# Kernel tuning notes

Hardware: AMD Instinct MI355X
Metric: run time of the kernel (lower is better)

Reference implementation:

```python
import jax, jax.numpy as jnp
import numpy as np

I, H, B, T = 5, 256, 4096, 256


def _lstm_layer(x, w_ih, w_hh, b_ih, b_hh):
    # x: [B, T, in]; precompute the input-side gate GEMM for all timesteps
    xg = jnp.einsum('bti,gi->btg', x, w_ih) + b_ih + b_hh  # [B, T, 4H]
    h0 = jnp.zeros((x.shape[0], H), x.dtype)
    c0 = jnp.zeros((x.shape[0], H), x.dtype)

    def step(carry, xg_t):
        h, c = carry
        g = xg_t + h @ w_hh.T                      # [B, 4H]
        i_g, f_g, g_g, o_g = jnp.split(g, 4, axis=-1)  # torch gate order i,f,g,o
        c = jax.nn.sigmoid(f_g) * c + jax.nn.sigmoid(i_g) * jnp.tanh(g_g)
        h = jax.nn.sigmoid(o_g) * jnp.tanh(c)
        return (h, c), h

    (_, _), hs = jax.lax.scan(step, (h0, c0), jnp.swapaxes(xg, 0, 1))  # hs: [T, B, H]
    return jnp.swapaxes(hs, 0, 1)  # [B, T, H]


def setup_inputs() -> dict:
    key = jax.random.key(0)
    ks = jax.random.split(key, 12)
    s = 1.0 / np.sqrt(H)
    u = lambda k, shape: jax.random.uniform(k, shape, jnp.float32, -s, s)
    return {
        'x': jax.random.normal(ks[0], (B, T, I), jnp.float32),
        'w_ih0': u(ks[1], (4 * H, I)),
        'w_hh0': u(ks[2], (4 * H, H)),
        'b_ih0': u(ks[3], (4 * H,)),
        'b_hh0': u(ks[4], (4 * H,)),
        'w_ih1': u(ks[5], (4 * H, H)),
        'w_hh1': u(ks[6], (4 * H, H)),
        'b_ih1': u(ks[7], (4 * H,)),
        'b_hh1': u(ks[8], (4 * H,)),
        'fc_w': u(ks[9], (1, H)),
        'fc_b': u(ks[10], (1,)),
    }


def reference(x, w_ih0, w_hh0, b_ih0, b_hh0, w_ih1, w_hh1, b_ih1, b_hh1, fc_w, fc_b):
    h1 = _lstm_layer(x, w_ih0, w_hh0, b_ih0, b_hh0)   # [B, T, H]
    # dropout between layers is identity in eval mode
    h2 = _lstm_layer(h1, w_ih1, w_hh1, b_ih1, b_hh1)  # [B, T, H]
    out = jnp.einsum('bth,oh->bto', h2, fc_w) + fc_b  # [B, T, 1]
    return out
```

## Files before the change

### kernel.cpp

```cpp
#include <hip/hip_runtime.h>

typedef unsigned short u16;
typedef _Float16 f16_t;
typedef f16_t f16x8 __attribute__((ext_vector_type(8)));
typedef float f32x4 __attribute__((ext_vector_type(4)));
typedef unsigned u32x4 __attribute__((ext_vector_type(4)));

#define T_STEPS 256
#define IN_DIM  5
#define NBLK    256

#define WS_BIAS 1638400
#define WS_FC   1646592
#define WS_GX   1654784
#define GXS     524288
#define WS_CNT  (WS_GX + 8388608)

__device__ __forceinline__ float sigf(float x)  { return 1.0f / (1.0f + __expf(-x)); }
__device__ __forceinline__ float tanh_f(float x){ return 1.0f - 2.0f / (__expf(2.0f * x) + 1.0f); }

__global__ void prep_kernel(const float* __restrict__ wih0, const float* __restrict__ whh0,
                            const float* __restrict__ wih1, const float* __restrict__ whh1,
                            const float* __restrict__ bih0, const float* __restrict__ bhh0,
                            const float* __restrict__ bih1, const float* __restrict__ bhh1,
                            const float* __restrict__ fcw,
                            u16* __restrict__ wsw, float* __restrict__ biases,
                            u16* __restrict__ wsfc, unsigned* __restrict__ cnt)
{
    int j = blockIdx.x * blockDim.x + threadIdx.x;
    if (j < 102400) {
        int slice = j / 3200;
        int rem   = j - slice * 3200;
        int f     = rem >> 6;
        int lane  = rem & 63;
        int sub = slice >> 2, wv = slice & 3;
        int lrow = lane & 15;
        int kp = (lane >> 4) * 8;
        int nt, ks; bool g0;
        if (f < 18) { g0 = true;  nt = f / 9;  ks = f - nt * 9; }
        else        { int ff = f - 18; g0 = false; nt = ff >> 4; ks = ff & 15; }
        int wr = (nt * 2 + (lrow >> 3)) * 256 + sub * 32 + wv * 8 + (lrow & 7);
        u16 tmp[8];
#pragma unroll
        for (int e = 0; e < 8; ++e) {
            int k = kp + e;
            float v;
            if (g0) {
                v = (ks < 8) ? whh0[wr * 256 + ks * 32 + k]
                             : (k < IN_DIM ? wih0[wr * IN_DIM + k] : 0.0f);
            } else {
                v = (ks < 8) ? wih1[wr * 256 + ks * 32 + k]
                             : whh1[wr * 256 + (ks - 8) * 32 + k];
            }
            tmp[e] = __builtin_bit_cast(u16, (f16_t)v);
        }
        *(uint4*)(wsw + (size_t)j * 8) = *(uint4*)tmp;
    } else if (j < 103424) {
        int i = j - 102400;
        biases[i] = bih0[i] + bhh0[i];
    } else if (j < 104448) {
        int i = j - 103424;
        biases[1024 + i] = bih1[i] + bhh1[i];
    } else if (j < 104960) {
        int q = j - 104448;
        int ks = q >> 6, lane = q & 63;
        u16 tmp[8];
#pragma unroll
        for (int e = 0; e < 8; ++e) {
            float v = ((lane & 15) == 0) ? fcw[ks * 32 + (lane >> 4) * 8 + e] : 0.0f;
            tmp[e] = __builtin_bit_cast(u16, (f16_t)v);
        }
        *(uint4*)(wsfc + (size_t)q * 8) = *(uint4*)tmp;
    } else if (j < 107008) {
        cnt[j - 104960] = 0u;
    }
}

__global__ __launch_bounds__(256, 1) void lstm_fused(
    const float* __restrict__ x, const u16* __restrict__ wsw,
    const float* __restrict__ biases, const u16* __restrict__ wsfc,
    const float* __restrict__ fcb_g, float* __restrict__ out,
    u16* __restrict__ gxbase, unsigned* __restrict__ cnt)
{
    extern __shared__ char smem[];
    char* h0A = smem;
    char* h1A = smem + 32768;
    char* xbA = smem + 65536;
    char* h0B = smem + 69632;
    char* h1B = smem + 102400;
    char* xbB = smem + 135168;

    const int tid  = threadIdx.x;
    const int wv   = tid >> 6;
    const int lane = tid & 63;
    const int lrow = lane & 15;
    const int lkg  = lane >> 4;
    const int hf   = lrow >> 3;
    const int cj   = lrow & 7;
    const int sub  = blockIdx.x >> 5;
    const int grp  = blockIdx.x & 31;
    const int r0   = grp * 128;
    const int aswz = (lrow & 7) << 4;
    const int xswz = (lrow & 3) << 4;

    f16x8 w0[2][9], w1[2][16], wfc[8];
    const u16* wbase = wsw + (size_t)(sub * 4 + wv) * 25600;
#pragma unroll
    for (int nt = 0; nt < 2; ++nt)
#pragma unroll
        for (int ks = 0; ks < 9; ++ks) {
            w0[nt][ks] = *(const f16x8*)(wbase + (nt * 9 + ks) * 512 + lane * 8);
            asm volatile("" : "+a"(w0[nt][ks]));
            __builtin_amdgcn_sched_barrier(0);
        }
#pragma unroll
    for (int nt = 0; nt < 2; ++nt)
#pragma unroll
        for (int ks = 0; ks < 16; ++ks) {
            w1[nt][ks] = *(const f16x8*)(wbase + (18 + nt * 16 + ks) * 512 + lane * 8);
            asm volatile("" : "+a"(w1[nt][ks]));
            __builtin_amdgcn_sched_barrier(0);
        }
#pragma unroll
    for (int ks = 0; ks < 8; ++ks) {
        wfc[ks] = *(const f16x8*)(wsfc + ks * 512 + lane * 8);
        asm volatile("" : "+a"(wfc[ks]));
        __builtin_amdgcn_sched_barrier(0);
    }

    float b0[2], b1[2];
#pragma unroll
    for (int nt = 0; nt < 2; ++nt) {
        int wr = (nt * 2 + hf) * 256 + sub * 32 + wv * 8 + cj;
        b0[nt] = biases[wr];
        b1[nt] = biases[1024 + wr];
    }
    const float fcb = fcb_g[0];

    unsigned* cA = cnt + grp * 16;
    unsigned* cB = cnt + 1024 + grp * 16;

    auto gxr = [&](int stream, int which, int parity) -> u16* {
        return gxbase + (size_t)((stream * 2 + which) * 2 + parity) * GXS + grp * 16384;
    };

    for (int i = tid; i < 139264 / 4; i += 256) ((unsigned*)smem)[i] = 0u;
    __syncthreads();
    {
        int i0 = tid, i1 = tid + 256;
        if (i0 < 320) { int row = i0 / 5, k = i0 - row * 5;
            float v = x[((size_t)(r0 + row) * T_STEPS + 0) * IN_DIM + k];
            *(u16*)(xbA + row * 64 + ((2 * k) ^ ((row & 3) << 4))) = __builtin_bit_cast(u16, (f16_t)v); }
        if (i1 < 320) { int row = i1 / 5, k = i1 - row * 5;
            float v = x[((size_t)(r0 + row) * T_STEPS + 0) * IN_DIM + k];
            *(u16*)(xbA + row * 64 + ((2 * k) ^ ((row & 3) << 4))) = __builtin_bit_cast(u16, (f16_t)v); }
    }
    __syncthreads();

    float c0A[4][2] = {}, c1A[4][2] = {}, c0B[4][2] = {}, c1B[4][2] = {};

    auto PUB = [&](u16* gxw, int mt, unsigned hv) {
        unsigned sh = __shfl_xor(hv, 1);
        int rowb = mt * 16 + lkg * 4 + hf * 2;
        unsigned word;
        if (cj & 1) { word = (sh >> 16) | (hv & 0xffff0000u); rowb += 1; }
        else        { word = (hv & 0xffffu) | (sh << 16); }
        int colp = wv * 8 + (cj & ~1);
        *(volatile unsigned*)((char*)gxw + sub * 4096 + rowb * 64 + colp * 2) = word;
    };

    auto GEMM0 = [&](const char* h0s, const char* xbs, float (&cs)[4][2], u16* gxw) {
#pragma unroll
        for (int mt = 0; mt < 4; ++mt) {
            f32x4 a0 = {}, a1 = {};
            const int arow = mt * 16 + lrow;
#pragma unroll
            for (int ks = 0; ks < 8; ++ks) {
                f16x8 a = *(const f16x8*)(h0s + arow * 512 + ((ks * 64 + lkg * 16) ^ aswz));
                a0 = __builtin_amdgcn_mfma_f32_16x16x32_f16(a, w0[0][ks], a0, 0, 0, 0);
                a1 = __builtin_amdgcn_mfma_f32_16x16x32_f16(a, w0[1][ks], a1, 0, 0, 0);
            }
            {
                f16x8 a = *(const f16x8*)(xbs + arow * 64 + ((lkg * 16) ^ xswz));
                a0 = __builtin_amdgcn_mfma_f32_16x16x32_f16(a, w0[0][8], a0, 0, 0, 0);
                a1 = __builtin_amdgcn_mfma_f32_16x16x32_f16(a, w0[1][8], a1, 0, 0, 0);
            }
#pragma unroll
            for (int r = 0; r < 4; ++r) { a0[r] += b0[0]; a1[r] += b0[1]; }
            float sA0 = __shfl_xor(hf ? a0[0] : a0[2], 8);
            float sA1 = __shfl_xor(hf ? a0[1] : a0[3], 8);
            float sB0 = __shfl_xor(hf ? a1[0] : a1[2], 8);
            float sB1 = __shfl_xor(hf ? a1[1] : a1[3], 8);
            unsigned hv = 0;
#pragma unroll
            for (int rr = 0; rr < 2; ++rr) {
                float sa = rr ? sA1 : sA0, sb = rr ? sB1 : sB0;
                float ig = hf ? sa : a0[rr];
                float fg = hf ? a0[2 + rr] : sa;
                float gg = hf ? sb : a1[rr];
                float og = hf ? a1[2 + rr] : sb;
                float c  = sigf(fg) * cs[mt][rr] + sigf(ig) * tanh_f(gg);
                cs[mt][rr] = c;
                float h  = sigf(og) * tanh_f(c);
                hv |= (unsigned)__builtin_bit_cast(u16, (f16_t)h) << (16 * rr);
            }
            PUB(gxw, mt, hv);
        }
    };
    auto GEMM1 = [&](const char* h0s, const char* h1s, float (&cs)[4][2], u16* gxw) {
#pragma unroll
        for (int mt = 0; mt < 4; ++mt) {
            f32x4 a0 = {}, a1 = {};
            const int arow = mt * 16 + lrow;
#pragma unroll
            for (int ks = 0; ks < 8; ++ks) {
                f16x8 a = *(const f16x8*)(h0s + arow * 512 + ((ks * 64 + lkg * 16) ^ aswz));
                a0 = __builtin_amdgcn_mfma_f32_16x16x32_f16(a, w1[0][ks], a0, 0, 0, 0);
                a1 = __builtin_amdgcn_mfma_f32_16x16x32_f16(a, w1[1][ks], a1, 0, 0, 0);
            }
#pragma unroll
            for (int ks = 0; ks < 8; ++ks) {
                f16x8 a = *(const f16x8*)(h1s + arow * 512 + ((ks * 64 + lkg * 16) ^ aswz));
                a0 = __builtin_amdgcn_mfma_f32_16x16x32_f16(a, w1[0][8 + ks], a0, 0, 0, 0);
                a1 = __builtin_amdgcn_mfma_f32_16x16x32_f16(a, w1[1][8 + ks], a1, 0, 0, 0);
            }
#pragma unroll
            for (int r = 0; r < 4; ++r) { a0[r] += b1[0]; a1[r] += b1[1]; }
            float sA0 = __shfl_xor(hf ? a0[0] : a0[2], 8);
            float sA1 = __shfl_xor(hf ? a0[1] : a0[3], 8);
            float sB0 = __shfl_xor(hf ? a1[0] : a1[2], 8);
            float sB1 = __shfl_xor(hf ? a1[1] : a1[3], 8);
            unsigned hv = 0;
#pragma unroll
            for (int rr = 0; rr < 2; ++rr) {
                float sa = rr ? sA1 : sA0, sb = rr ? sB1 : sB0;
                float ig = hf ? sa : a0[rr];
                float fg = hf ? a0[2 + rr] : sa;
                float gg = hf ? sb : a1[rr];
                float og = hf ? a1[2 + rr] : sb;
                float c  = sigf(fg) * cs[mt][rr] + sigf(ig) * tanh_f(gg);
                cs[mt][rr] = c;
                float h  = sigf(og) * tanh_f(c);
                hv |= (unsigned)__builtin_bit_cast(u16, (f16_t)h) << (16 * rr);
            }
            PUB(gxw, mt, hv);
        }
    };
    auto REL = [&](unsigned* p) {
        if (tid == 0)
            __hip_atomic_fetch_add(p, 1u, __ATOMIC_RELAXED, __HIP_MEMORY_SCOPE_AGENT);
    };
    auto SPIN = [&](unsigned* p, unsigned tgt) {
        if (tid == 0) {
            while (__hip_atomic_load(p, __ATOMIC_RELAXED, __HIP_MEMORY_SCOPE_AGENT) < tgt)
                __builtin_amdgcn_s_sleep(1);
        }
        __syncthreads();
    };
    auto FILL2 = [&](char* d0, const u16* s0, bool e0,
                     char* d1, const u16* s1, bool e1) {
        u32x4 q0[8], q1[8];
        const int row = tid & 63;
        const int base = (tid >> 6) * 2;
#pragma unroll
        for (int ss = 0; ss < 2; ++ss) {
            int s2 = base + ss;
            if (e0) {
                const char* sp = (const char*)s0 + s2 * 4096 + row * 64;
#pragma unroll
                for (int j = 0; j < 4; ++j)
                    asm volatile("global_load_dwordx4 %0, %1, off sc0 sc1"
                                 : "=&v"(q0[ss * 4 + j]) : "v"(sp + j * 16));
            }
            if (e1) {
                const char* sp = (const char*)s1 + s2 * 4096 + row * 64;
#pragma unroll
                for (int j = 0; j < 4; ++j)
                    asm volatile("global_load_dwordx4 %0, %1, off sc0 sc1"
                                 : "=&v"(q1[ss * 4 + j]) : "v"(sp + j * 16));
            }
        }
        asm volatile("s_waitcnt vmcnt(0)" ::: "memory");
        __builtin_amdgcn_sched_barrier(0);
        const int sw = (row & 7) << 4;
#pragma unroll
        for (int ss = 0; ss < 2; ++ss) {
            int s2 = base + ss;
            if (e0) {
#pragma unroll
                for (int j = 0; j < 4; ++j)
                    *(u32x4*)(d0 + row * 512 + ((s2 * 64 + j * 16) ^ sw)) = q0[ss * 4 + j];
            }
            if (e1) {
#pragma unroll
                for (int j = 0; j < 4; ++j)
                    *(u32x4*)(d1 + row * 512 + ((s2 * 64 + j * 16) ^ sw)) = q1[ss * 4 + j];
            }
        }
    };
    auto XLOAD = [&](int strOff, int tt, float& v0, float& v1) {
        v0 = 0.f; v1 = 0.f;
        int i0 = tid, i1 = tid + 256;
        if (i0 < 320) { int row = i0 / 5, k = i0 - row * 5;
            v0 = x[((size_t)(r0 + strOff + row) * T_STEPS + tt) * IN_DIM + k]; }
        if (i1 < 320) { int row = i1 / 5, k = i1 - row * 5;
            v1 = x[((size_t)(r0 + strOff + row) * T_STEPS + tt) * IN_DIM + k]; }
    };
    auto XSTAGE = [&](char* xbs, float v0, float v1) {
        int i0 = tid, i1 = tid + 256;
        if (i0 < 320) { int row = i0 / 5, k = i0 - row * 5;
            *(u16*)(xbs + row * 64 + ((2 * k) ^ ((row & 3) << 4))) = __builtin_bit_cast(u16, (f16_t)v0); }
        if (i1 < 320) { int row = i1 / 5, k = i1 - row * 5;
            *(u16*)(xbs + row * 64 + ((2 * k) ^ ((row & 3) << 4))) = __builtin_bit_cast(u16, (f16_t)v1); }
    };
    auto FC = [&](const char* h1s, int strOff, int tIdx, bool mine, int sub4) {
        if (wv == 0 && mine) {
            f32x4 acc = {};
            const int arow = sub4 * 16 + lrow;
#pragma unroll
            for (int ks = 0; ks < 8; ++ks) {
                f16x8 a = *(const f16x8*)(h1s + arow * 512 + ((ks * 64 + lkg * 16) ^ aswz));
                acc = __builtin_amdgcn_mfma_f32_16x16x32_f16(a, wfc[ks], acc, 0, 0, 0);
            }
            if (lrow == 0) {
#pragma unroll
                for (int r = 0; r < 4; ++r)
                    out[(size_t)(r0 + strOff + sub4 * 16 + lkg * 4 + r) * T_STEPS + tIdx] = acc[r] + fcb;
            }
        }
    };

#pragma unroll 1
    for (int t = 0; t < T_STEPS; ++t) {
        const int pc = t & 1, pp = (t - 1) & 1;

        float xa0, xa1, xbv0, xbv1;
        if (t + 1 < T_STEPS) { XLOAD(0, t + 1, xa0, xa1); } else { xa0 = 0.f; xa1 = 0.f; }
        XLOAD(64, t, xbv0, xbv1);

        GEMM0(h0A, xbA, c0A, gxr(0, 0, pc));
        if (t > 0) GEMM1(h0A, h1A, c1A, gxr(0, 1, pp));

        SPIN(cB, 8u * (unsigned)t);
        FILL2(h0B, gxr(1, 0, pp), t > 0,
              h1B, gxr(1, 1, pc), t > 1);
        XSTAGE(xbB, xbv0, xbv1);
        __syncthreads();
        REL(cA);
        if (t > 1) FC(h1B, 64, t - 2, sub >= 4, sub - 4);

        GEMM0(h0B, xbB, c0B, gxr(1, 0, pc));
        if (t > 0) GEMM1(h0B, h1B, c1B, gxr(1, 1, pp));

        SPIN(cA, 8u * (unsigned)(t + 1));
        FILL2(h0A, gxr(0, 0, pc), true,
              h1A, gxr(0, 1, pp), t > 0);
        if (t + 1 < T_STEPS) XSTAGE(xbA, xa0, xa1);
        __syncthreads();
        REL(cB);
        if (t > 0) FC(h1A, 0, t - 1, sub < 4, sub);
    }

    GEMM1(h0A, h1A, c1A, gxr(0, 1, 1));
    SPIN(cB, 8u * 256u);
    FILL2(h0B, gxr(1, 0, 1), true,
          h1B, gxr(1, 1, 0), true);
    __syncthreads();
    REL(cA);
    FC(h1B, 64, 254, sub >= 4, sub - 4);
    GEMM1(h0B, h1B, c1B, gxr(1, 1, 1));
    SPIN(cA, 8u * 257u);
    FILL2(h1A, gxr(0, 1, 1), true, h1A, gxr(0, 1, 1), false);
    __syncthreads();
    REL(cB);
    FC(h1A, 0, 255, sub < 4, sub);
    SPIN(cB, 8u * 257u);
    FILL2(h1B, gxr(1, 1, 1), true, h1B, gxr(1, 1, 1), false);
    __syncthreads();
    FC(h1B, 64, 255, sub >= 4, sub - 4);
}

extern "C" void kernel_launch(void* const* d_in, const int* in_sizes, int n_in,
                              void* d_out, int out_size, void* d_ws, size_t ws_size,
                              hipStream_t stream)
{
    const float* x    = (const float*)d_in[0];
    const float* wih0 = (const float*)d_in[1];
    const float* whh0 = (const float*)d_in[2];
    const float* bih0 = (const float*)d_in[3];
    const float* bhh0 = (const float*)d_in[4];
    const float* wih1 = (const float*)d_in[5];
    const float* whh1 = (const float*)d_in[6];
    const float* bih1 = (const float*)d_in[7];
    const float* bhh1 = (const float*)d_in[8];
    const float* fcw  = (const float*)d_in[9];
    const float* fcb  = (const float*)d_in[10];

    u16* wsw      = (u16*)d_ws;
    float* biases = (float*)((char*)d_ws + WS_BIAS);
    u16* wsfc     = (u16*)((char*)d_ws + WS_FC);
    u16* gxbase   = (u16*)((char*)d_ws + WS_GX);
    unsigned* cnt = (unsigned*)((char*)d_ws + WS_CNT);

    prep_kernel<<<419, 256, 0, stream>>>(wih0, whh0, wih1, whh1,
                                         bih0, bhh0, bih1, bhh1, fcw,
                                         wsw, biases, wsfc, cnt);
    lstm_fused<<<NBLK, 256, 139264, stream>>>(x, wsw, biases, wsfc, fcb,
                                              (float*)d_out, gxbase, cnt);
}
```

Measured before the change: 5.715 ms.

## Split LSTM gate columns across eight waves per block instead of four

Doubles the block to 512 threads so each wave owns one 16-column gate tile (4 hidden units × 4 gates) instead of two. The prep kernel's weight layout is reorganised to match. The gate epilogue now gathers i/f/g/o across lanes with two rounds of shuffles, each wave fills one h sub-slice, and the FC weights move from registers into LDS. The aim is to shorten each wave's serial MFMA and epilogue chain inside the latency-bound timestep loop and hide latency with more waves. The cost is extra shuffles and higher register pressure under the tighter launch bounds.

```diff
diff --git a/kernel.cpp b/kernel.cpp
--- a/kernel.cpp
+++ b/kernel.cpp
@@ -29,28 +29,27 @@
 {
     int j = blockIdx.x * blockDim.x + threadIdx.x;
     if (j < 102400) {
-        int slice = j / 3200;
-        int rem   = j - slice * 3200;
+        int slice = j / 1600;
+        int rem   = j - slice * 1600;
         int f     = rem >> 6;
         int lane  = rem & 63;
-        int sub = slice >> 2, wv = slice & 3;
+        int sub = slice >> 3, w = slice & 7;
         int lrow = lane & 15;
+        int g = lrow >> 2, c4 = lrow & 3;
+        int wr = g * 256 + sub * 32 + w * 4 + c4;
         int kp = (lane >> 4) * 8;
-        int nt, ks; bool g0;
-        if (f < 18) { g0 = true;  nt = f / 9;  ks = f - nt * 9; }
-        else        { int ff = f - 18; g0 = false; nt = ff >> 4; ks = ff & 15; }
-        int wr = (nt * 2 + (lrow >> 3)) * 256 + sub * 32 + wv * 8 + (lrow & 7);
         u16 tmp[8];
 #pragma unroll
         for (int e = 0; e < 8; ++e) {
             int k = kp + e;
             float v;
-            if (g0) {
-                v = (ks < 8) ? whh0[wr * 256 + ks * 32 + k]
-                             : (k < IN_DIM ? wih0[wr * IN_DIM + k] : 0.0f);
+            if (f < 9) {
+                v = (f < 8) ? whh0[wr * 256 + f * 32 + k]
+                            : (k < IN_DIM ? wih0[wr * IN_DIM + k] : 0.0f);
             } else {
-                v = (ks < 8) ? wih1[wr * 256 + ks * 32 + k]
-                             : whh1[wr * 256 + (ks - 8) * 32 + k];
+                int ff = f - 9;
+                v = (ff < 8) ? wih1[wr * 256 + ff * 32 + k]
+                             : whh1[wr * 256 + (ff - 8) * 32 + k];
             }
             tmp[e] = __builtin_bit_cast(u16, (f16_t)v);
         }
@@ -76,65 +75,52 @@
     }
 }
 
-__global__ __launch_bounds__(256, 1) void lstm_fused(
+__global__ __launch_bounds__(512, 2) void lstm_fused(
     const float* __restrict__ x, const u16* __restrict__ wsw,
     const float* __restrict__ biases, const u16* __restrict__ wsfc,
     const float* __restrict__ fcb_g, float* __restrict__ out,
     u16* __restrict__ gxbase, unsigned* __restrict__ cnt)
 {
     extern __shared__ char smem[];
-    char* h0A = smem;
-    char* h1A = smem + 32768;
-    char* xbA = smem + 65536;
-    char* h0B = smem + 69632;
-    char* h1B = smem + 102400;
-    char* xbB = smem + 135168;
+    char* h0A  = smem;
+    char* h1A  = smem + 32768;
+    char* xbA  = smem + 65536;
+    char* h0B  = smem + 69632;
+    char* h1B  = smem + 102400;
+    char* xbB  = smem + 135168;
+    char* wfcL = smem + 139264;
 
     const int tid  = threadIdx.x;
-    const int wv   = tid >> 6;
+    const int wvv  = tid >> 6;
     const int lane = tid & 63;
     const int lrow = lane & 15;
     const int lkg  = lane >> 4;
-    const int hf   = lrow >> 3;
-    const int cj   = lrow & 7;
+    const int g    = lrow >> 2;
+    const int c4   = lrow & 3;
     const int sub  = blockIdx.x >> 5;
     const int grp  = blockIdx.x & 31;
     const int r0   = grp * 128;
     const int aswz = (lrow & 7) << 4;
     const int xswz = (lrow & 3) << 4;
 
-    f16x8 w0[2][9], w1[2][16], wfc[8];
-    const u16* wbase = wsw + (size_t)(sub * 4 + wv) * 25600;
-#pragma unroll
-    for (int nt = 0; nt < 2; ++nt)
-#pragma unroll
-        for (int ks = 0; ks < 9; ++ks) {
-            w0[nt][ks] = *(const f16x8*)(wbase + (nt * 9 + ks) * 512 + lane * 8);
-            asm volatile("" : "+a"(w0[nt][ks]));
-            __builtin_amdgcn_sched_barrier(0);
-        }
-#pragma unroll
-    for (int nt = 0; nt < 2; ++nt)
-#pragma unroll
-        for (int ks = 0; ks < 16; ++ks) {
-            w1[nt][ks] = *(const f16x8*)(wbase + (18 + nt * 16 + ks) * 512 + lane * 8);
-            asm volatile("" : "+a"(w1[nt][ks]));
-            __builtin_amdgcn_sched_barrier(0);
-        }
-#pragma unroll
-    for (int ks = 0; ks < 8; ++ks) {
-        wfc[ks] = *(const f16x8*)(wsfc + ks * 512 + lane * 8);
-        asm volatile("" : "+a"(wfc[ks]));
+    f16x8 w0[9], w1[16];
+    const u16* wbase = wsw + (size_t)(sub * 8 + wvv) * 12800;
+#pragma unroll
+    for (int ks = 0; ks < 9; ++ks) {
+        w0[ks] = *(const f16x8*)(wbase + ks * 512 + lane * 8);
+        asm volatile("" : "+a"(w0[ks]));
         __builtin_amdgcn_sched_barrier(0);
     }
-
-    float b0[2], b1[2];
-#pragma unroll
-    for (int nt = 0; nt < 2; ++nt) {
-        int wr = (nt * 2 + hf) * 256 + sub * 32 + wv * 8 + cj;
-        b0[nt] = biases[wr];
-        b1[nt] = biases[1024 + wr];
-    }
+#pragma unroll
+    for (int ks = 0; ks < 16; ++ks) {
+        w1[ks] = *(const f16x8*)(wbase + (9 + ks) * 512 + lane * 8);
+        asm volatile("" : "+a"(w1[ks]));
+        __builtin_amdgcn_sched_barrier(0);
+    }
+
+    const int colglob = sub * 32 + wvv * 4 + c4;
+    const float b0s = biases[g * 256 + colglob];
+    const float b1s = biases[1024 + g * 256 + colglob];
     const float fcb = fcb_g[0];
 
     unsigned* cA = cnt + grp * 16;
@@ -144,106 +130,73 @@
         return gxbase + (size_t)((stream * 2 + which) * 2 + parity) * GXS + grp * 16384;
     };
 
-    for (int i = tid; i < 139264 / 4; i += 256) ((unsigned*)smem)[i] = 0u;
-    __syncthreads();
-    {
-        int i0 = tid, i1 = tid + 256;
-        if (i0 < 320) { int row = i0 / 5, k = i0 - row * 5;
-            float v = x[((size_t)(r0 + row) * T_STEPS + 0) * IN_DIM + k];
-            *(u16*)(xbA + row * 64 + ((2 * k) ^ ((row & 3) << 4))) = __builtin_bit_cast(u16, (f16_t)v); }
-        if (i1 < 320) { int row = i1 / 5, k = i1 - row * 5;
-            float v = x[((size_t)(r0 + row) * T_STEPS + 0) * IN_DIM + k];
-            *(u16*)(xbA + row * 64 + ((2 * k) ^ ((row & 3) << 4))) = __builtin_bit_cast(u16, (f16_t)v); }
-    }
-    __syncthreads();
-
-    float c0A[4][2] = {}, c1A[4][2] = {}, c0B[4][2] = {}, c1B[4][2] = {};
-
-    auto PUB = [&](u16* gxw, int mt, unsigned hv) {
+    for (int i = tid; i < 147456 / 4; i += 512) ((unsigned*)smem)[i] = 0u;
+    __syncthreads();
+    *(uint4*)(wfcL + tid * 16) = *(const uint4*)(wsfc + tid * 8);
+    if (tid < 320) {
+        int row = tid / 5, k = tid - row * 5;
+        float v = x[((size_t)(r0 + row) * T_STEPS + 0) * IN_DIM + k];
+        *(u16*)(xbA + row * 64 + ((2 * k) ^ ((row & 3) << 4))) = __builtin_bit_cast(u16, (f16_t)v);
+    }
+    __syncthreads();
+
+    float c0A[4] = {}, c1A[4] = {}, c0B[4] = {}, c1B[4] = {};
+
+    auto EPI = [&](f32x4 ac, float bias, float& cs, u16* gxw, int mt) {
+        float v[4];
+#pragma unroll
+        for (int r = 0; r < 4; ++r) v[r] = ac[r] + bias;
+        float e1 = __shfl_xor(v[(g & 1) ? 0 : 1], 4);
+        float e2 = __shfl_xor(v[(g & 1) ? 2 : 3], 4);
+        if (g & 1) { v[0] = e1; v[2] = e2; } else { v[1] = e1; v[3] = e2; }
+        float f1 = __shfl_xor(v[(g & 2) ? 0 : 2], 8);
+        float f2 = __shfl_xor(v[(g & 2) ? 1 : 3], 8);
+        if (g & 2) { v[0] = f1; v[1] = f2; } else { v[2] = f1; v[3] = f2; }
+        float c = sigf(v[1]) * cs + sigf(v[0]) * tanh_f(v[2]);
+        cs = c;
+        float h = sigf(v[3]) * tanh_f(c);
+        unsigned hv = (unsigned)__builtin_bit_cast(u16, (f16_t)h);
         unsigned sh = __shfl_xor(hv, 1);
-        int rowb = mt * 16 + lkg * 4 + hf * 2;
-        unsigned word;
-        if (cj & 1) { word = (sh >> 16) | (hv & 0xffff0000u); rowb += 1; }
-        else        { word = (hv & 0xffffu) | (sh << 16); }
-        int colp = wv * 8 + (cj & ~1);
-        *(volatile unsigned*)((char*)gxw + sub * 4096 + rowb * 64 + colp * 2) = word;
-    };
-
-    auto GEMM0 = [&](const char* h0s, const char* xbs, float (&cs)[4][2], u16* gxw) {
+        if (!(lane & 1)) {
+            int row = mt * 16 + lkg * 4 + g;
+            *(volatile unsigned*)((char*)gxw + sub * 4096 + row * 64 + (wvv * 4 + c4) * 2)
+                = hv | (sh << 16);
+        }
+    };
+
+    auto GEMM0 = [&](const char* h0s, const char* xbs, float (&cs)[4], u16* gxw) {
 #pragma unroll
         for (int mt = 0; mt < 4; ++mt) {
-            f32x4 a0 = {}, a1 = {};
+            f32x4 ac = {};
             const int arow = mt * 16 + lrow;
 #pragma unroll
             for (int ks = 0; ks < 8; ++ks) {
                 f16x8 a = *(const f16x8*)(h0s + arow * 512 + ((ks * 64 + lkg * 16) ^ aswz));
-                a0 = __builtin_amdgcn_mfma_f32_16x16x32_f16(a, w0[0][ks], a0, 0, 0, 0);
-                a1 = __builtin_amdgcn_mfma_f32_16x16x32_f16(a, w0[1][ks], a1, 0, 0, 0);
+                ac = __builtin_amdgcn_mfma_f32_16x16x32_f16(a, w0[ks], ac, 0, 0, 0);
             }
             {
                 f16x8 a = *(const f16x8*)(xbs + arow * 64 + ((lkg * 16) ^ xswz));
-                a0 = __builtin_amdgcn_mfma_f32_16x16x32_f16(a, w0[0][8], a0, 0, 0, 0);
-                a1 = __builtin_amdgcn_mfma_f32_16x16x32_f16(a, w0[1][8], a1, 0, 0, 0);
-            }
-#pragma unroll
-            for (int r = 0; r < 4; ++r) { a0[r] += b0[0]; a1[r] += b0[1]; }
-            float sA0 = __shfl_xor(hf ? a0[0] : a0[2], 8);
-            float sA1 = __shfl_xor(hf ? a0[1] : a0[3], 8);
-            float sB0 = __shfl_xor(hf ? a1[0] : a1[2], 8);
-            float sB1 = __shfl_xor(hf ? a1[1] : a1[3], 8);
-            unsigned hv = 0;
-#pragma unroll
-            for (int rr = 0; rr < 2; ++rr) {
-                float sa = rr ? sA1 : sA0, sb = rr ? sB1 : sB0;
-                float ig = hf ? sa : a0[rr];
-                float fg = hf ? a0[2 + rr] : sa;
-                float gg = hf ? sb : a1[rr];
-                float og = hf ? a1[2 + rr] : sb;
-                float c  = sigf(fg) * cs[mt][rr] + sigf(ig) * tanh_f(gg);
-                cs[mt][rr] = c;
-                float h  = sigf(og) * tanh_f(c);
-                hv |= (unsigned)__builtin_bit_cast(u16, (f16_t)h) << (16 * rr);
-            }
-            PUB(gxw, mt, hv);
-        }
-    };
-    auto GEMM1 = [&](const char* h0s, const char* h1s, float (&cs)[4][2], u16* gxw) {
+                ac = __builtin_amdgcn_mfma_f32_16x16x32_f16(a, w0[8], ac, 0, 0, 0);
+            }
+            EPI(ac, b0s, cs[mt], gxw, mt);
+        }
+    };
+    auto GEMM1 = [&](const char* h0s, const char* h1s, float (&cs)[4], u16* gxw) {
 #pragma unroll
         for (int mt = 0; mt < 4; ++mt) {
-            f32x4 a0 = {}, a1 = {};
+            f32x4 ac = {};
             const int arow = mt * 16 + lrow;
 #pragma unroll
             for (int ks = 0; ks < 8; ++ks) {
                 f16x8 a = *(const f16x8*)(h0s + arow * 512 + ((ks * 64 + lkg * 16) ^ aswz));
-                a0 = __builtin_amdgcn_mfma_f32_16x16x32_f16(a, w1[0][ks], a0, 0, 0, 0);
-                a1 = __builtin_amdgcn_mfma_f32_16x16x32_f16(a, w1[1][ks], a1, 0, 0, 0);
+                ac = __builtin_amdgcn_mfma_f32_16x16x32_f16(a, w1[ks], ac, 0, 0, 0);
             }
 #pragma unroll
             for (int ks = 0; ks < 8; ++ks) {
                 f16x8 a = *(const f16x8*)(h1s + arow * 512 + ((ks * 64 + lkg * 16) ^ aswz));
-                a0 = __builtin_amdgcn_mfma_f32_16x16x32_f16(a, w1[0][8 + ks], a0, 0, 0, 0);
-                a1 = __builtin_amdgcn_mfma_f32_16x16x32_f16(a, w1[1][8 + ks], a1, 0, 0, 0);
-            }
-#pragma unroll
-            for (int r = 0; r < 4; ++r) { a0[r] += b1[0]; a1[r] += b1[1]; }
-            float sA0 = __shfl_xor(hf ? a0[0] : a0[2], 8);
-            float sA1 = __shfl_xor(hf ? a0[1] : a0[3], 8);
-            float sB0 = __shfl_xor(hf ? a1[0] : a1[2], 8);
-            float sB1 = __shfl_xor(hf ? a1[1] : a1[3], 8);
-            unsigned hv = 0;
-#pragma unroll
-            for (int rr = 0; rr < 2; ++rr) {
-                float sa = rr ? sA1 : sA0, sb = rr ? sB1 : sB0;
-                float ig = hf ? sa : a0[rr];
-                float fg = hf ? a0[2 + rr] : sa;
-                float gg = hf ? sb : a1[rr];
-                float og = hf ? a1[2 + rr] : sb;
-                float c  = sigf(fg) * cs[mt][rr] + sigf(ig) * tanh_f(gg);
-                cs[mt][rr] = c;
-                float h  = sigf(og) * tanh_f(c);
-                hv |= (unsigned)__builtin_bit_cast(u16, (f16_t)h) << (16 * rr);
-            }
-            PUB(gxw, mt, hv);
+                ac = __builtin_amdgcn_mfma_f32_16x16x32_f16(a, w1[8 + ks], ac, 0, 0, 0);
+            }
+            EPI(ac, b1s, cs[mt], gxw, mt);
         }
     };
     auto REL = [&](unsigned* p) {
@@ -259,68 +212,54 @@
     };
     auto FILL2 = [&](char* d0, const u16* s0, bool e0,
                      char* d1, const u16* s1, bool e1) {
-        u32x4 q0[8], q1[8];
-        const int row = tid & 63;
-        const int base = (tid >> 6) * 2;
-#pragma unroll
-        for (int ss = 0; ss < 2; ++ss) {
-            int s2 = base + ss;
-            if (e0) {
-                const char* sp = (const char*)s0 + s2 * 4096 + row * 64;
-#pragma unroll
-                for (int j = 0; j < 4; ++j)
-                    asm volatile("global_load_dwordx4 %0, %1, off sc0 sc1"
-                                 : "=&v"(q0[ss * 4 + j]) : "v"(sp + j * 16));
-            }
-            if (e1) {
-                const char* sp = (const char*)s1 + s2 * 4096 + row * 64;
-#pragma unroll
-                for (int j = 0; j < 4; ++j)
-                    asm volatile("global_load_dwordx4 %0, %1, off sc0 sc1"
-                                 : "=&v"(q1[ss * 4 + j]) : "v"(sp + j * 16));
-            }
+        u32x4 q0[4], q1[4];
+        const int row = lane;
+        if (e0) {
+            const char* sp = (const char*)s0 + wvv * 4096 + row * 64;
+#pragma unroll
+            for (int j = 0; j < 4; ++j)
+                asm volatile("global_load_dwordx4 %0, %1, off sc0 sc1"
+                             : "=&v"(q0[j]) : "v"(sp + j * 16));
+        }
+        if (e1) {
+            const char* sp = (const char*)s1 + wvv * 4096 + row * 64;
+#pragma unroll
+            for (int j = 0; j < 4; ++j)
+                asm volatile("global_load_dwordx4 %0, %1, off sc0 sc1"
+                             : "=&v"(q1[j]) : "v"(sp + j * 16));
         }
         asm volatile("s_waitcnt vmcnt(0)" ::: "memory");
         __builtin_amdgcn_sched_barrier(0);
         const int sw = (row & 7) << 4;
-#pragma unroll
-        for (int ss = 0; ss < 2; ++ss) {
-            int s2 = base + ss;
-            if (e0) {
-#pragma unroll
-                for (int j = 0; j < 4; ++j)
-                    *(u32x4*)(d0 + row * 512 + ((s2 * 64 + j * 16) ^ sw)) = q0[ss * 4 + j];
-            }
-            if (e1) {
-#pragma unroll
-                for (int j = 0; j < 4; ++j)
-                    *(u32x4*)(d1 + row * 512 + ((s2 * 64 + j * 16) ^ sw)) = q1[ss * 4 + j];
-            }
-        }
-    };
-    auto XLOAD = [&](int strOff, int tt, float& v0, float& v1) {
-        v0 = 0.f; v1 = 0.f;
-        int i0 = tid, i1 = tid + 256;
-        if (i0 < 320) { int row = i0 / 5, k = i0 - row * 5;
+        if (e0) {
+#pragma unroll
+            for (int j = 0; j < 4; ++j)
+                *(u32x4*)(d0 + row * 512 + ((wvv * 64 + j * 16) ^ sw)) = q0[j];
+        }
+        if (e1) {
+#pragma unroll
+            for (int j = 0; j < 4; ++j)
+                *(u32x4*)(d1 + row * 512 + ((wvv * 64 + j * 16) ^ sw)) = q1[j];
+        }
+    };
+    auto XLOAD = [&](int strOff, int tt, float& v0) {
+        v0 = 0.f;
+        if (tid < 320) { int row = tid / 5, k = tid - row * 5;
             v0 = x[((size_t)(r0 + strOff + row) * T_STEPS + tt) * IN_DIM + k]; }
-        if (i1 < 320) { int row = i1 / 5, k = i1 - row * 5;
-            v1 = x[((size_t)(r0 + strOff + row) * T_STEPS + tt) * IN_DIM + k]; }
-    };
-    auto XSTAGE = [&](char* xbs, float v0, float v1) {
-        int i0 = tid, i1 = tid + 256;
-        if (i0 < 320) { int row = i0 / 5, k = i0 - row * 5;
+    };
+    auto XSTAGE = [&](char* xbs, float v0) {
+        if (tid < 320) { int row = tid / 5, k = tid - row * 5;
             *(u16*)(xbs + row * 64 + ((2 * k) ^ ((row & 3) << 4))) = __builtin_bit_cast(u16, (f16_t)v0); }
-        if (i1 < 320) { int row = i1 / 5, k = i1 - row * 5;
-            *(u16*)(xbs + row * 64 + ((2 * k) ^ ((row & 3) << 4))) = __builtin_bit_cast(u16, (f16_t)v1); }
     };
     auto FC = [&](const char* h1s, int strOff, int tIdx, bool mine, int sub4) {
-        if (wv == 0 && mine) {
+        if (wvv == 0 && mine) {
             f32x4 acc = {};
             const int arow = sub4 * 16 + lrow;
 #pragma unroll
             for (int ks = 0; ks < 8; ++ks) {
                 f16x8 a = *(const f16x8*)(h1s + arow * 512 + ((ks * 64 + lkg * 16) ^ aswz));
-                acc = __builtin_amdgcn_mfma_f32_16x16x32_f16(a, wfc[ks], acc, 0, 0, 0);
+                f16x8 wb = *(const f16x8*)(wfcL + ks * 1024 + lane * 16);
+                acc = __builtin_amdgcn_mfma_f32_16x16x32_f16(a, wb, acc, 0, 0, 0);
             }
             if (lrow == 0) {
 #pragma unroll
@@ -334,9 +273,9 @@
     for (int t = 0; t < T_STEPS; ++t) {
         const int pc = t & 1, pp = (t - 1) & 1;
 
-        float xa0, xa1, xbv0, xbv1;
-        if (t + 1 < T_STEPS) { XLOAD(0, t + 1, xa0, xa1); } else { xa0 = 0.f; xa1 = 0.f; }
-        XLOAD(64, t, xbv0, xbv1);
+        float xa0, xbv0;
+        if (t + 1 < T_STEPS) { XLOAD(0, t + 1, xa0); } else { xa0 = 0.f; }
+        XLOAD(64, t, xbv0);
 
         GEMM0(h0A, xbA, c0A, gxr(0, 0, pc));
         if (t > 0) GEMM1(h0A, h1A, c1A, gxr(0, 1, pp));
@@ -344,7 +283,7 @@
         SPIN(cB, 8u * (unsigned)t);
         FILL2(h0B, gxr(1, 0, pp), t > 0,
               h1B, gxr(1, 1, pc), t > 1);
-        XSTAGE(xbB, xbv0, xbv1);
+        XSTAGE(xbB, xbv0);
         __syncthreads();
         REL(cA);
         if (t > 1) FC(h1B, 64, t - 2, sub >= 4, sub - 4);
@@ -355,7 +294,7 @@
         SPIN(cA, 8u * (unsigned)(t + 1));
         FILL2(h0A, gxr(0, 0, pc), true,
               h1A, gxr(0, 1, pp), t > 0);
-        if (t + 1 < T_STEPS) XSTAGE(xbA, xa0, xa1);
+        if (t + 1 < T_STEPS) XSTAGE(xbA, xa0);
         __syncthreads();
         REL(cB);
         if (t > 0) FC(h1A, 0, t - 1, sub < 4, sub);
@@ -405,6 +344,6 @@
     prep_kernel<<<419, 256, 0, stream>>>(wih0, whh0, wih1, whh1,
                                          bih0, bhh0, bih1, bhh1, fcw,
                                          wsw, biases, wsfc, cnt);
-    lstm_fused<<<NBLK, 256, 139264, stream>>>(x, wsw, biases, wsfc, fcb,
+    lstm_fused<<<NBLK, 512, 147456, stream>>>(x, wsw, biases, wsfc, fcb,
                                               (float*)d_out, gxbase, cnt);
 }
```

Result: slower. 5.871 ms (+2.7%).

## Replace atomic counters with per-block step flags and vectorize hidden-state publish stores

Applied to the files above, without the earlier changes.

Inter-block synchronization previously used a shared atomic counter per group, incremented after each fill and polled by one thread. Now each block writes its own step flag with a plain store right after its GEMMs, and a whole wave polls the eight peer flags in parallel. Hidden-state publishing is changed from per-lane 4-byte stores to lane shuffles that assemble 16-byte rows, written by a quarter of the lanes. The aim is to cut atomic contention, release flags earlier, and reduce the number of global store transactions, at the cost of extra shuffles and an added __syncthreads before each release.

```diff
diff --git a/kernel.cpp b/kernel.cpp
--- a/kernel.cpp
+++ b/kernel.cpp
@@ -137,8 +137,10 @@
     }
     const float fcb = fcb_g[0];
 
-    unsigned* cA = cnt + grp * 16;
-    unsigned* cB = cnt + 1024 + grp * 16;
+    unsigned* fA    = cnt + grp * 8;
+    unsigned* fB    = cnt + 256 + grp * 8;
+    unsigned* fAme  = fA + sub;
+    unsigned* fBme  = fB + sub;
 
     auto gxr = [&](int stream, int which, int parity) -> u16* {
         return gxbase + (size_t)((stream * 2 + which) * 2 + parity) * GXS + grp * 16384;
@@ -161,15 +163,27 @@
 
     auto PUB = [&](u16* gxw, int mt, unsigned hv) {
         unsigned sh = __shfl_xor(hv, 1);
-        int rowb = mt * 16 + lkg * 4 + hf * 2;
-        unsigned word;
-        if (cj & 1) { word = (sh >> 16) | (hv & 0xffff0000u); rowb += 1; }
-        else        { word = (hv & 0xffffu) | (sh << 16); }
-        int colp = wv * 8 + (cj & ~1);
-        *(volatile unsigned*)((char*)gxw + sub * 4096 + rowb * 64 + colp * 2) = word;
-    };
-
-    auto GEMM0 = [&](const char* h0s, const char* xbs, float (&cs)[4][2], u16* gxw) {
+        const int rsel = cj & 1;
+        unsigned w01;
+        if (rsel) w01 = (sh >> 16) | (hv & 0xffff0000u);
+        else      w01 = (hv & 0xffffu) | (sh << 16);
+        unsigned p2 = __shfl_xor(w01, 2);
+        unsigned lo4, hi4;
+        if (cj & 2) { lo4 = p2;  hi4 = w01; }
+        else        { lo4 = w01; hi4 = p2;  }
+        unsigned q0 = __shfl_xor(lo4, 4), q1 = __shfl_xor(hi4, 4);
+        u32x4 full;
+        if (cj & 4) { full[0] = q0;  full[1] = q1;  full[2] = lo4; full[3] = hi4; }
+        else        { full[0] = lo4; full[1] = hi4; full[2] = q0;  full[3] = q1;  }
+        if (cj < 2) {
+            int row = mt * 16 + lkg * 4 + hf * 2 + rsel;
+            char* ap = (char*)gxw + sub * 4096 + row * 64 + wv * 16;
+            asm volatile("global_store_dwordx4 %0, %1, off sc0 sc1"
+                         :: "v"(ap), "v"(full) : "memory");
+        }
+    };
+
+    auto GEMM0x = [&](const char* h0s, const char* xbs, float (&cs)[4][2], u16* gxw) {
 #pragma unroll
         for (int mt = 0; mt < 4; ++mt) {
             f32x4 a0 = {}, a1 = {};
@@ -207,7 +221,7 @@
             PUB(gxw, mt, hv);
         }
     };
-    auto GEMM1 = [&](const char* h0s, const char* h1s, float (&cs)[4][2], u16* gxw) {
+    auto GEMM1x = [&](const char* h0s, const char* h1s, float (&cs)[4][2], u16* gxw) {
 #pragma unroll
         for (int mt = 0; mt < 4; ++mt) {
             f32x4 a0 = {}, a1 = {};
@@ -246,14 +260,23 @@
             PUB(gxw, mt, hv);
         }
     };
-    auto REL = [&](unsigned* p) {
+    auto RELF = [&](unsigned* fme, unsigned val) {
         if (tid == 0)
-            __hip_atomic_fetch_add(p, 1u, __ATOMIC_RELAXED, __HIP_MEMORY_SCOPE_AGENT);
-    };
-    auto SPIN = [&](unsigned* p, unsigned tgt) {
-        if (tid == 0) {
-            while (__hip_atomic_load(p, __ATOMIC_RELAXED, __HIP_MEMORY_SCOPE_AGENT) < tgt)
+            asm volatile("global_store_dword %0, %1, off sc0 sc1"
+                         :: "v"(fme), "v"(val) : "memory");
+    };
+    auto SPINF = [&](unsigned* f, unsigned tgt) {
+        if (wv == 0) {
+            while (true) {
+                unsigned v = tgt;
+                if (lane < 8)
+                    asm volatile("global_load_dword %0, %1, off sc0 sc1\n\t"
+                                 "s_waitcnt vmcnt(0)"
+                                 : "=v"(v) : "v"(f + lane) : "memory");
+                bool ok = (lane >= 8) || (v >= tgt);
+                if (__all(ok)) break;
                 __builtin_amdgcn_s_sleep(1);
+            }
         }
         __syncthreads();
     };
@@ -338,43 +361,47 @@
         if (t + 1 < T_STEPS) { XLOAD(0, t + 1, xa0, xa1); } else { xa0 = 0.f; xa1 = 0.f; }
         XLOAD(64, t, xbv0, xbv1);
 
-        GEMM0(h0A, xbA, c0A, gxr(0, 0, pc));
-        if (t > 0) GEMM1(h0A, h1A, c1A, gxr(0, 1, pp));
-
-        SPIN(cB, 8u * (unsigned)t);
+        GEMM0x(h0A, xbA, c0A, gxr(0, 0, pc));
+        if (t > 0) GEMM1x(h0A, h1A, c1A, gxr(0, 1, pp));
+        __syncthreads();
+        RELF(fAme, (unsigned)(t + 1));
+
+        SPINF(fB, (unsigned)t);
         FILL2(h0B, gxr(1, 0, pp), t > 0,
               h1B, gxr(1, 1, pc), t > 1);
         XSTAGE(xbB, xbv0, xbv1);
         __syncthreads();
-        REL(cA);
         if (t > 1) FC(h1B, 64, t - 2, sub >= 4, sub - 4);
 
-        GEMM0(h0B, xbB, c0B, gxr(1, 0, pc));
-        if (t > 0) GEMM1(h0B, h1B, c1B, gxr(1, 1, pp));
-
-        SPIN(cA, 8u * (unsigned)(t + 1));
+        GEMM0x(h0B, xbB, c0B, gxr(1, 0, pc));
+        if (t > 0) GEMM1x(h0B, h1B, c1B, gxr(1, 1, pp));
+        __syncthreads();
+        RELF(fBme, (unsigned)(t + 1));
+
+        SPINF(fA, (unsigned)(t + 1));
         FILL2(h0A, gxr(0, 0, pc), true,
               h1A, gxr(0, 1, pp), t > 0);
         if (t + 1 < T_STEPS) XSTAGE(xbA, xa0, xa1);
         __syncthreads();
-        REL(cB);
         if (t > 0) FC(h1A, 0, t - 1, sub < 4, sub);
     }
 
-    GEMM1(h0A, h1A, c1A, gxr(0, 1, 1));
-    SPIN(cB, 8u * 256u);
+    GEMM1x(h0A, h1A, c1A, gxr(0, 1, 1));
+    __syncthreads();
+    RELF(fAme, 257u);
+    SPINF(fB, 256u);
     FILL2(h0B, gxr(1, 0, 1), true,
           h1B, gxr(1, 1, 0), true);
     __syncthreads();
-    REL(cA);
     FC(h1B, 64, 254, sub >= 4, sub - 4);
-    GEMM1(h0B, h1B, c1B, gxr(1, 1, 1));
-    SPIN(cA, 8u * 257u);
+    GEMM1x(h0B, h1B, c1B, gxr(1, 1, 1));
+    __syncthreads();
+    RELF(fBme, 257u);
+    SPINF(fA, 257u);
     FILL2(h1A, gxr(0, 1, 1), true, h1A, gxr(0, 1, 1), false);
     __syncthreads();
-    REL(cB);
     FC(h1A, 0, 255, sub < 4, sub);
-    SPIN(cB, 8u * 257u);
+    SPINF(fB, 257u);
     FILL2(h1B, gxr(1, 1, 1), true, h1B, gxr(1, 1, 1), false);
     __syncthreads();
     FC(h1B, 64, 255, sub >= 4, sub - 4);
```

Measured after the change: 4.899 ms. -14.3%, faster.
